# Performance work log

Measured on AMD Instinct MI355X. Metric: run time of the kernel, lower is better.

The kernel has to match this reference:

```python
import jax, jax.numpy as jnp
import numpy as np

NUM_DOTS = 100
IMG_SIZE = 4096


def setup_inputs() -> dict:
    key = jax.random.key(0)
    k1, k2, k3, k4 = jax.random.split(key, 4)
    adv_patch = jax.random.uniform(k1, (3, IMG_SIZE, IMG_SIZE), dtype=jnp.float32)
    centers = jax.random.uniform(k2, (NUM_DOTS, 2), dtype=jnp.float32)
    radii = jax.random.uniform(k3, (NUM_DOTS,), dtype=jnp.float32)
    colors = jax.random.uniform(k4, (NUM_DOTS, 3), dtype=jnp.float32)
    return {"adv_patch": adv_patch, "centers": centers, "radii": radii, "colors": colors}


def reference(adv_patch, centers, radii, colors):
    # Replicates PatchTrainer.forward: for each dot, draw a filled circle
    # (PIL ellipse with center (int(cx*S), int(cy*S)) and radius int(r*S/5))
    # and overwrite the three channels with the dot's color inside the circle.
    # Later dots overwrite earlier ones (sequential masked_fill_), so we scan.
    S = adv_patch.shape[-1]
    # int() truncation on non-negative values == floor
    xc = jnp.floor(centers[:, 0] * S)          # [N] horizontal center (image x)
    yc = jnp.floor(centers[:, 1] * S)          # [N] vertical center (image y)
    r = jnp.floor(radii * (S / 5.0))           # [N]
    xs = jnp.arange(S, dtype=adv_patch.dtype)  # columns (x)
    ys = jnp.arange(S, dtype=adv_patch.dtype)  # rows (y)

    def step(patch, dot):
        xci, yci, ri, col = dot
        # circle mask [S, S] indexed [y, x], matching ToTensor() layout
        d2 = (xs[None, :] - xci) ** 2 + (ys[:, None] - yci) ** 2
        mask = d2 <= ri * ri
        patch = jnp.where(mask[None, :, :], col[:, None, None], patch)
        return patch, None

    out, _ = jax.lax.scan(step, adv_patch, (xc, yc, r, colors))
    return out
```

## Files before the change

### kernel.cpp

```cpp
#include <hip/hip_runtime.h>


#define IMG  4096
#define ND   100
#define TW   256
#define TH   32

typedef float vfloat4 __attribute__((ext_vector_type(4)));

__global__ __launch_bounds__(256) void patch_dots_kernel(
    const float* __restrict__ patch,
    const float* __restrict__ centers,
    const float* __restrict__ radii,
    const float* __restrict__ colors,
    float* __restrict__ out)
{
    __shared__ float  s_xc[ND], s_yc[ND], s_r2[ND];
    __shared__ float4 s_col[ND];
    __shared__ int    s_list[ND];
    __shared__ unsigned long long s_mask[2];
    __shared__ int    s_cnt;

    const int tx0 = blockIdx.x * TW;
    const int ty0 = blockIdx.y * TH;
    const int t   = threadIdx.x;
    const int lane = t & 63;
    const int w    = t >> 6;

    int flag = 0;
    if (t < ND) {
        float xc = floorf(centers[2 * t]     * 4096.0f);
        float yc = floorf(centers[2 * t + 1] * 4096.0f);
        float r  = floorf(radii[t] * (4096.0f / 5.0f));
        float r2 = r * r;
        s_xc[t] = xc; s_yc[t] = yc; s_r2[t] = r2;
        s_col[t] = make_float4(colors[3 * t], colors[3 * t + 1], colors[3 * t + 2], 0.f);
        float cx = fminf(fmaxf(xc, (float)tx0), (float)(tx0 + TW - 1));
        float cy = fminf(fmaxf(yc, (float)ty0), (float)(ty0 + TH - 1));
        float dx = xc - cx, dy = yc - cy;
        flag = (dx * dx + dy * dy <= r2) ? 1 : 0;
    }
    if (t < 128) {
        unsigned long long m = __ballot(flag != 0);
        if (lane == 0) s_mask[w] = m;
    }
    __syncthreads();
    {
        const unsigned long long m0 = s_mask[0];
        if (flag) {
            const unsigned long long mw = s_mask[w];
            int pos = __popcll(mw & ((1ull << lane) - 1)) + (w ? __popcll(m0) : 0);
            s_list[pos] = t;
        }
        if (t == 0) s_cnt = __popcll(m0) + __popcll(s_mask[1]);
    }
    __syncthreads();
    const int cnt = s_cnt;

    const int x0   = tx0 + lane * 4;
    const float fx0 = (float)x0;
    const float fx1 = (float)(x0 + 1);
    const float fx2 = (float)(x0 + 2);
    const float fx3 = (float)(x0 + 3);

    for (int it = 0; it < TH / 4; ++it) {
        const int   y  = ty0 + it * 4 + w;
        const float fy = (float)y;

        int b0 = -1, b1 = -1, b2 = -1, b3 = -1;
        for (int k = cnt - 1; k >= 0; --k) {
            const int   i  = s_list[k];
            const float dy = fy - s_yc[i];
            const float t2 = s_r2[i] - dy * dy;
            if (t2 < 0.f) continue;
            const float xc = s_xc[i];
            const float dx0 = fx0 - xc;
            const float dx1 = fx1 - xc;
            const float dx2 = fx2 - xc;
            const float dx3 = fx3 - xc;
            if (b0 < 0 && dx0 * dx0 <= t2) b0 = i;
            if (b1 < 0 && dx1 * dx1 <= t2) b1 = i;
            if (b2 < 0 && dx2 * dx2 <= t2) b2 = i;
            if (b3 < 0 && dx3 * dx3 <= t2) b3 = i;
            if (__all((b0 | b1 | b2 | b3) >= 0)) break;
        }

        const size_t base = (size_t)y * IMG + x0;

        float4 p0 = make_float4(0.f, 0.f, 0.f, 0.f);
        float4 p1 = p0, p2 = p0;
        if ((b0 | b1 | b2 | b3) < 0) {
            p0 = *(const float4*)(patch + base);
            p1 = *(const float4*)(patch + base + (size_t)IMG * IMG);
            p2 = *(const float4*)(patch + base + 2 * (size_t)IMG * IMG);
        }

        const float4 c0 = (b0 >= 0) ? s_col[b0] : make_float4(p0.x, p1.x, p2.x, 0.f);
        const float4 c1 = (b1 >= 0) ? s_col[b1] : make_float4(p0.y, p1.y, p2.y, 0.f);
        const float4 c2 = (b2 >= 0) ? s_col[b2] : make_float4(p0.z, p1.z, p2.z, 0.f);
        const float4 c3 = (b3 >= 0) ? s_col[b3] : make_float4(p0.w, p1.w, p2.w, 0.f);

        vfloat4 o0, o1, o2;
        o0.x = c0.x; o0.y = c1.x; o0.z = c2.x; o0.w = c3.x;
        o1.x = c0.y; o1.y = c1.y; o1.z = c2.y; o1.w = c3.y;
        o2.x = c0.z; o2.y = c1.z; o2.z = c2.z; o2.w = c3.z;

        *(vfloat4*)(out + base)                          = o0;
        *(vfloat4*)(out + base + (size_t)IMG * IMG)      = o1;
        *(vfloat4*)(out + base + 2 * (size_t)IMG * IMG)  = o2;
    }
}

extern "C" void kernel_launch(void* const* d_in, const int* in_sizes, int n_in,
                              void* d_out, int out_size, void* d_ws, size_t ws_size,
                              hipStream_t stream) {
    const float* patch   = (const float*)d_in[0];
    const float* centers = (const float*)d_in[1];
    const float* radii   = (const float*)d_in[2];
    const float* colors  = (const float*)d_in[3];
    float* out = (float*)d_out;

    dim3 grid(IMG / TW, IMG / TH);
    dim3 block(256);
    patch_dots_kernel<<<grid, block, 0, stream>>>(patch, centers, radii, colors, out);
}
```

Measured before the change: 310.4 us.

## Split work per color channel across a 1D grid of blocks

Launches three times as many blocks, each handling a single color channel of a tile, so every block does one load and one store per pixel group instead of three. The circle-coverage search runs three times as often in exchange. Memory parallelism rises and per-thread register pressure falls. The 1D grid walks x fastest, then y, then channel, which changes DRAM access locality.

```diff
diff --git a/kernel.cpp b/kernel.cpp
--- a/kernel.cpp
+++ b/kernel.cpp
@@ -5,6 +5,8 @@
 #define ND   100
 #define TW   256
 #define TH   32
+#define NBX  (IMG / TW)
+#define NBY  (IMG / TH)
 
 typedef float vfloat4 __attribute__((ext_vector_type(4)));
 
@@ -15,17 +17,23 @@
     const float* __restrict__ colors,
     float* __restrict__ out)
 {
-    __shared__ float  s_xc[ND], s_yc[ND], s_r2[ND];
-    __shared__ float4 s_col[ND];
+    __shared__ float  s_xc[ND], s_yc[ND], s_r2[ND], s_col[ND];
     __shared__ int    s_list[ND];
     __shared__ unsigned long long s_mask[2];
     __shared__ int    s_cnt;
 
-    const int tx0 = blockIdx.x * TW;
-    const int ty0 = blockIdx.y * TH;
+    const int bid = blockIdx.x;
+    const int bx  = bid % NBX;
+    const int by  = (bid / NBX) % NBY;
+    const int z   = bid / (NBX * NBY);
+
+    const int tx0 = bx * TW;
+    const int ty0 = by * TH;
     const int t   = threadIdx.x;
     const int lane = t & 63;
     const int w    = t >> 6;
+
+    const size_t plane = (size_t)z * IMG * IMG;
 
     int flag = 0;
     if (t < ND) {
@@ -34,7 +42,7 @@
         float r  = floorf(radii[t] * (4096.0f / 5.0f));
         float r2 = r * r;
         s_xc[t] = xc; s_yc[t] = yc; s_r2[t] = r2;
-        s_col[t] = make_float4(colors[3 * t], colors[3 * t + 1], colors[3 * t + 2], 0.f);
+        s_col[t] = colors[3 * t + z];
         float cx = fminf(fmaxf(xc, (float)tx0), (float)(tx0 + TW - 1));
         float cy = fminf(fmaxf(yc, (float)ty0), (float)(ty0 + TH - 1));
         float dx = xc - cx, dy = yc - cy;
@@ -85,29 +93,19 @@
             if (__all((b0 | b1 | b2 | b3) >= 0)) break;
         }
 
-        const size_t base = (size_t)y * IMG + x0;
+        const size_t base = plane + (size_t)y * IMG + x0;
 
-        float4 p0 = make_float4(0.f, 0.f, 0.f, 0.f);
-        float4 p1 = p0, p2 = p0;
-        if ((b0 | b1 | b2 | b3) < 0) {
-            p0 = *(const float4*)(patch + base);
-            p1 = *(const float4*)(patch + base + (size_t)IMG * IMG);
-            p2 = *(const float4*)(patch + base + 2 * (size_t)IMG * IMG);
-        }
+        float4 p = make_float4(0.f, 0.f, 0.f, 0.f);
+        if ((b0 | b1 | b2 | b3) < 0)
+            p = *(const float4*)(patch + base);
 
-        const float4 c0 = (b0 >= 0) ? s_col[b0] : make_float4(p0.x, p1.x, p2.x, 0.f);
-        const float4 c1 = (b1 >= 0) ? s_col[b1] : make_float4(p0.y, p1.y, p2.y, 0.f);
-        const float4 c2 = (b2 >= 0) ? s_col[b2] : make_float4(p0.z, p1.z, p2.z, 0.f);
-        const float4 c3 = (b3 >= 0) ? s_col[b3] : make_float4(p0.w, p1.w, p2.w, 0.f);
+        vfloat4 o;
+        o.x = (b0 >= 0) ? s_col[b0] : p.x;
+        o.y = (b1 >= 0) ? s_col[b1] : p.y;
+        o.z = (b2 >= 0) ? s_col[b2] : p.z;
+        o.w = (b3 >= 0) ? s_col[b3] : p.w;
 
-        vfloat4 o0, o1, o2;
-        o0.x = c0.x; o0.y = c1.x; o0.z = c2.x; o0.w = c3.x;
-        o1.x = c0.y; o1.y = c1.y; o1.z = c2.y; o1.w = c3.y;
-        o2.x = c0.z; o2.y = c1.z; o2.z = c2.z; o2.w = c3.z;
-
-        *(vfloat4*)(out + base)                          = o0;
-        *(vfloat4*)(out + base + (size_t)IMG * IMG)      = o1;
-        *(vfloat4*)(out + base + 2 * (size_t)IMG * IMG)  = o2;
+        *(vfloat4*)(out + base) = o;
     }
 }
 
@@ -120,7 +118,7 @@
     const float* colors  = (const float*)d_in[3];
     float* out = (float*)d_out;
 
-    dim3 grid(IMG / TW, IMG / TH);
+    dim3 grid(NBX * NBY * 3);
     dim3 block(256);
     patch_dots_kernel<<<grid, block, 0, stream>>>(patch, centers, radii, colors, out);
 }
```

Result: no change. 308.3 us (-0.7%).
